# Optimization experiments

Measured on AMD Instinct MI355X. Metric: run time of the kernel, lower is better.

The kernel has to match this reference:

```python
import jax, jax.numpy as jnp
import numpy as np

N, F, H, K_SUB, DEPTH = 500_000, 64, 32, 16, 4
N_NODES = 2 ** DEPTH - 1   # 15 internal nodes
N_LEAVES = 2 ** DEPTH      # 16 leaves
SLOPE = 0.01               # torch LeakyReLU default negative_slope


def _leaky(v):
    return jnp.where(v >= 0, v, SLOPE * v)


def setup_inputs() -> dict:
    key = jax.random.key(0)
    ks = jax.random.split(key, 8)
    x = jax.random.normal(ks[0], (N, F), dtype=jnp.float32)
    subset_idx = jax.random.randint(ks[1], (N_NODES, K_SUB), 0, F, dtype=jnp.int32)
    W1 = jax.random.normal(ks[2], (N_NODES, H, K_SUB), dtype=jnp.float32) * (1.0 / np.sqrt(K_SUB))
    b1 = jnp.zeros((N_NODES, H), jnp.float32)
    W2 = jax.random.normal(ks[3], (N_NODES, H, H), dtype=jnp.float32) * (1.0 / np.sqrt(H))
    b2 = jnp.zeros((N_NODES, H), jnp.float32)
    W3 = jax.random.normal(ks[4], (N_NODES, 2, H), dtype=jnp.float32) * (1.0 / np.sqrt(H))
    b3 = jnp.zeros((N_NODES, 2), jnp.float32)
    # leaf 'best' constants (class modes precomputed by populate_best)
    leaf_best = jax.random.randint(ks[5], (N_LEAVES,), 0, 10).astype(jnp.float32)
    return {"x": x, "W1": W1, "b1": b1, "W2": W2, "b2": b2, "W3": W3, "b3": b3,
            "leaf_best": leaf_best, "subset_idx": subset_idx}


def _forward(x, W1, b1, W2, b2, W3, b3, leaf_best, subset_idx):
    n = x.shape[0]
    loc = jnp.zeros((n,), jnp.int32)   # local node index within current level
    off = 0
    for level in range(DEPTH):
        k = 2 ** level
        sl = slice(off, off + k)
        xs = x[:, subset_idx[sl]]                                   # [N, k, K_SUB]
        h = _leaky(jnp.einsum('nkf,khf->nkh', xs, W1[sl]) + b1[sl])  # [N, k, H]
        h = _leaky(jnp.einsum('nkh,kgh->nkg', h, W2[sl]) + b2[sl])   # [N, k, H]
        logits = jnp.einsum('nkh,koh->nko', h, W3[sl]) + b3[sl]      # [N, k, 2]
        p0 = jax.nn.softmax(logits, axis=-1)[..., 0]                 # [N, k]
        p0_row = jnp.take_along_axis(p0, loc[:, None], axis=1)[:, 0]
        bit = (p0_row < 0.5).astype(jnp.int32)  # 0 -> left, 1 -> right
        loc = 2 * loc + bit
        off += k
    return leaf_best[loc]  # [N]


def reference(x, W1, b1, W2, b2, W3, b3, leaf_best, subset_idx):
    return _forward(x, W1, b1, W2, b2, W3, b3, leaf_best, subset_idx)
```

## Files before the change

kernel.cpp:

```cpp
#include <hip/hip_runtime.h>

#define NF 64
#define NH 32
#define NK 16
#define NNODES 15
#define BLOCK 512
#define NWAVES (BLOCK / 64)
#define SPB (2 * BLOCK)


__global__ __attribute__((amdgpu_flat_work_group_size(BLOCK, BLOCK),
                          amdgpu_waves_per_eu(2, 4)))
void tree_mlp_kernel(
    const float* __restrict__ x,
    const float* __restrict__ W1, const float* __restrict__ b1,
    const float* __restrict__ W2, const float* __restrict__ b2,
    const float* __restrict__ W3, const float* __restrict__ b3,
    const float* __restrict__ leaf_best, const int* __restrict__ subset_idx,
    float* __restrict__ out, int N)
{
    __shared__ __align__(16) float W2Lv[8 * 1024];
    __shared__ int      subL[NNODES * NK];
    __shared__ unsigned permL[SPB];
    __shared__ int      sortL[64];

    const int tid  = threadIdx.x;
    const int lane = tid & 63;
    const int wv   = tid >> 6;
    const unsigned long long lt =
        (lane == 0) ? 0ull : ((~0ull) >> (64 - lane));

    for (int i = tid; i < NNODES * NK; i += BLOCK) subL[i] = subset_idx[i];
    {
        const float4* src = (const float4*)W2;
        float4* dst = (float4*)W2Lv;
        for (int i = tid; i < 256; i += BLOCK) dst[i] = src[i];
    }
    __syncthreads();

    const int base = blockIdx.x * SPB;
    int idA = base + tid;
    int idB = base + BLOCK + tid;
    int vA = (idA < N) ? 1 : 0; if (!vA) idA = 0;
    int vB = (idB < N) ? 1 : 0; if (!vB) idB = 0;
    int locA = 0, locB = 0, off = 0;

    #pragma unroll 1
    for (int level = 0; level < 4; ++level) {
        if (level > 0) {
            const int nb = 1 << level;
            int rkA = 0, rkB = 0;
            #pragma unroll 1
            for (int b = 0; b < nb; ++b) {
                const unsigned long long mA = __ballot(locA == b);
                const unsigned long long mB = __ballot(locB == b);
                if (locA == b) rkA = __popcll(mA & lt);
                if (locB == b) rkB = __popcll(mA) + __popcll(mB & lt);
                if (lane == 0)
                    sortL[b * NWAVES + wv] = __popcll(mA) + __popcll(mB);
            }
            __syncthreads();

            {
                const int cnt4 = (1 << level) * 256;
                const float4* src = (const float4*)(W2 + (size_t)off * 1024);
                float4* dst = (float4*)W2Lv;
                for (int i = tid; i < cnt4; i += BLOCK) dst[i] = src[i];
            }
            if (wv == 0) {
                const int cnt = nb * NWAVES;
                int v = (lane < cnt) ? sortL[lane] : 0;
                int incl = v;
                #pragma unroll
                for (int d = 1; d < 64; d <<= 1) {
                    int t = __shfl_up(incl, d, 64);
                    if (lane >= d) incl += t;
                }
                if (lane < cnt) sortL[lane] = incl - v;
            }
            __syncthreads();

            const int slotA = sortL[locA * NWAVES + wv] + rkA;
            const int slotB = sortL[locB * NWAVES + wv] + rkB;
            permL[slotA] = ((unsigned)idA << 5) | ((unsigned)vA << 4) | (unsigned)locA;
            permL[slotB] = ((unsigned)idB << 5) | ((unsigned)vB << 4) | (unsigned)locB;
            __syncthreads();
            const unsigned pA = permL[wv * 128 + 2 * lane];
            const unsigned pB = permL[wv * 128 + 2 * lane + 1];
            idA = (int)(pA >> 5); vA = (int)((pA >> 4) & 1u); locA = (int)(pA & 15u);
            idB = (int)(pB >> 5); vB = (int)((pB >> 4) & 1u); locB = (int)(pB & 15u);
            __syncthreads();
        }

        const int nodeA = off + locA;
        const int nodeB = off + locB;
        int bitA, bitB;

        if (__all(nodeA == nodeB)) {
            const int* si = subL + nodeA * NK;
            const float* xrA = x + (size_t)idA * NF;
            const float* xrB = x + (size_t)idB * NF;
            float xsA[NK], xsB[NK];
            #pragma unroll
            for (int k = 0; k < NK; ++k) {
                const int f = si[k];
                xsA[k] = xrA[f];
                xsB[k] = xrB[f];
            }

            float h1A[NH], h1B[NH];
            {
                const float4* w1g = (const float4*)(W1 + nodeA * (NH * NK));
                const float*  b1g = b1 + nodeA * NH;
                #pragma unroll
                for (int j = 0; j < NH; ++j) {
                    const float bj = b1g[j];
                    float aA = bj, aB = bj;
                    #pragma unroll
                    for (int q = 0; q < NK / 4; ++q) {
                        const float4 t = w1g[j * 4 + q];
                        aA += t.x * xsA[q * 4 + 0]; aB += t.x * xsB[q * 4 + 0];
                        aA += t.y * xsA[q * 4 + 1]; aB += t.y * xsB[q * 4 + 1];
                        aA += t.z * xsA[q * 4 + 2]; aB += t.z * xsB[q * 4 + 2];
                        aA += t.w * xsA[q * 4 + 3]; aB += t.w * xsB[q * 4 + 3];
                    }
                    h1A[j] = (aA >= 0.f) ? aA : 0.01f * aA;
                    h1B[j] = (aB >= 0.f) ? aB : 0.01f * aB;
                }
            }

            const float* w2l = W2Lv + (locA << 10);
            const float* bb2 = b2 + nodeA * NH;
            const float* w3g = W3 + nodeA * 2 * NH;
            const float bi0 = b3[nodeA * 2 + 0];
            const float bi1 = b3[nodeA * 2 + 1];
            float l0A = bi0, l1A = bi1, l0B = bi0, l1B = bi1;

            #pragma unroll 2
            for (int g = 0; g < NH; ++g) {
                const float bg = bb2[g];
                float aA = bg, aB = bg;
                const float4* row = (const float4*)(w2l + g * NH);
                #pragma unroll
                for (int q = 0; q < NH / 4; ++q) {
                    const float4 t = row[q];
                    aA += t.x * h1A[q * 4 + 0]; aB += t.x * h1B[q * 4 + 0];
                    aA += t.y * h1A[q * 4 + 1]; aB += t.y * h1B[q * 4 + 1];
                    aA += t.z * h1A[q * 4 + 2]; aB += t.z * h1B[q * 4 + 2];
                    aA += t.w * h1A[q * 4 + 3]; aB += t.w * h1B[q * 4 + 3];
                }
                const float h2A = (aA >= 0.f) ? aA : 0.01f * aA;
                const float h2B = (aB >= 0.f) ? aB : 0.01f * aB;
                const float wa = w3g[g];
                const float wb = w3g[NH + g];
                l0A += wa * h2A; l1A += wb * h2A;
                l0B += wa * h2B; l1B += wb * h2B;
            }
            bitA = (l0A < l1A) ? 1 : 0;
            bitB = (l0B < l1B) ? 1 : 0;
        } else {
            #pragma unroll 1
            for (int s2 = 0; s2 < 2; ++s2) {
                const int idS  = s2 ? idB : idA;
                const int locS = s2 ? locB : locA;
                const int node = off + locS;
                const int* si = subL + node * NK;
                const float* xr = x + (size_t)idS * NF;
                float xs[NK];
                #pragma unroll
                for (int k = 0; k < NK; ++k) xs[k] = xr[si[k]];

                float h1v[NH];
                const float4* w1g = (const float4*)(W1 + node * (NH * NK));
                const float*  b1g = b1 + node * NH;
                #pragma unroll
                for (int j = 0; j < NH; ++j) {
                    float acc = b1g[j];
                    #pragma unroll
                    for (int q = 0; q < NK / 4; ++q) {
                        const float4 t = w1g[j * 4 + q];
                        acc += t.x * xs[q * 4 + 0];
                        acc += t.y * xs[q * 4 + 1];
                        acc += t.z * xs[q * 4 + 2];
                        acc += t.w * xs[q * 4 + 3];
                    }
                    h1v[j] = (acc >= 0.f) ? acc : 0.01f * acc;
                }

                const float* w2l = W2Lv + (locS << 10);
                const float* bb2 = b2 + node * NH;
                const float* w3g = W3 + node * 2 * NH;
                float l0 = b3[node * 2 + 0];
                float l1 = b3[node * 2 + 1];
                #pragma unroll 2
                for (int g = 0; g < NH; ++g) {
                    float acc = bb2[g];
                    const float4* row = (const float4*)(w2l + g * NH);
                    #pragma unroll
                    for (int q = 0; q < NH / 4; ++q) {
                        const float4 t = row[q];
                        acc += t.x * h1v[q * 4 + 0];
                        acc += t.y * h1v[q * 4 + 1];
                        acc += t.z * h1v[q * 4 + 2];
                        acc += t.w * h1v[q * 4 + 3];
                    }
                    const float h2 = (acc >= 0.f) ? acc : 0.01f * acc;
                    l0 += w3g[g]      * h2;
                    l1 += w3g[NH + g] * h2;
                }
                const int bit = (l0 < l1) ? 1 : 0;
                if (s2) bitB = bit; else bitA = bit;
            }
        }

        locA = 2 * locA + bitA;
        locB = 2 * locB + bitB;
        off = 2 * off + 1;
    }

    if (vA) out[idA] = leaf_best[locA];
    if (vB) out[idB] = leaf_best[locB];
}

extern "C" void kernel_launch(void* const* d_in, const int* in_sizes, int n_in,
                              void* d_out, int out_size, void* d_ws, size_t ws_size,
                              hipStream_t stream) {
    const float* x         = (const float*)d_in[0];
    const float* W1        = (const float*)d_in[1];
    const float* b1        = (const float*)d_in[2];
    const float* W2        = (const float*)d_in[3];
    const float* b2        = (const float*)d_in[4];
    const float* W3        = (const float*)d_in[5];
    const float* b3        = (const float*)d_in[6];
    const float* leaf_best = (const float*)d_in[7];
    const int*   subset    = (const int*)d_in[8];

    const int N = in_sizes[0] / NF;
    const int grid = (N + SPB - 1) / SPB;
    tree_mlp_kernel<<<grid, BLOCK, 0, stream>>>(
        x, W1, b1, W2, b2, W3, b3, leaf_best, subset, (float*)d_out, N);
}
```

Baseline: 434.3 us.

## Pad per-node sort buckets to even size so sample pairs share a node

Each block now processes 1008 samples instead of 1024. The bucket sort pads every node group to an even length by inserting a dummy slot, so each thread's A/B sample pair always belongs to the same node. This removes the divergent serial fallback path and the per-level __all check, so the paired compute path always runs. In exchange, blocks do slightly less real work, padding slots are computed as invalid samples, and a small extra scan computes the pad offsets.

```diff
diff --git a/kernel.cpp b/kernel.cpp
--- a/kernel.cpp
+++ b/kernel.cpp
@@ -6,7 +6,8 @@
 #define NNODES 15
 #define BLOCK 512
 #define NWAVES (BLOCK / 64)
-#define SPB (2 * BLOCK)
+#define SPB 1008
+#define PSLOTS (1024 + 16)
 
 
 __global__ __attribute__((amdgpu_flat_work_group_size(BLOCK, BLOCK),
@@ -21,8 +22,9 @@
 {
     __shared__ __align__(16) float W2Lv[8 * 1024];
     __shared__ int      subL[NNODES * NK];
-    __shared__ unsigned permL[SPB];
+    __shared__ __align__(8) unsigned permL[PSLOTS];
     __shared__ int      sortL[64];
+    __shared__ int      padL[8];
 
     const int tid  = threadIdx.x;
     const int lane = tid & 63;
@@ -41,21 +43,22 @@
     const int base = blockIdx.x * SPB;
     int idA = base + tid;
     int idB = base + BLOCK + tid;
-    int vA = (idA < N) ? 1 : 0; if (!vA) idA = 0;
-    int vB = (idB < N) ? 1 : 0; if (!vB) idB = 0;
+    int vA = (idA < N) ? 1 : 0;                      if (!vA) idA = 0;
+    int vB = (tid < SPB - BLOCK && idB < N) ? 1 : 0; if (!vB) idB = 0;
     int locA = 0, locB = 0, off = 0;
 
     #pragma unroll 1
     for (int level = 0; level < 4; ++level) {
         if (level > 0) {
             const int nb = 1 << level;
+            *(unsigned long long*)(permL + 2 * tid) = 0ull;
             int rkA = 0, rkB = 0;
             #pragma unroll 1
             for (int b = 0; b < nb; ++b) {
-                const unsigned long long mA = __ballot(locA == b);
-                const unsigned long long mB = __ballot(locB == b);
-                if (locA == b) rkA = __popcll(mA & lt);
-                if (locB == b) rkB = __popcll(mA) + __popcll(mB & lt);
+                const unsigned long long mA = __ballot(vA && locA == b);
+                const unsigned long long mB = __ballot(vB && locB == b);
+                if (vA && locA == b) rkA = __popcll(mA & lt);
+                if (vB && locB == b) rkB = __popcll(mA) + __popcll(mB & lt);
                 if (lane == 0)
                     sortL[b * NWAVES + wv] = __popcll(mA) + __popcll(mB);
             }
@@ -77,27 +80,44 @@
                     if (lane >= d) incl += t;
                 }
                 if (lane < cnt) sortL[lane] = incl - v;
-            }
-            __syncthreads();
-
-            const int slotA = sortL[locA * NWAVES + wv] + rkA;
-            const int slotB = sortL[locB * NWAVES + wv] + rkB;
-            permL[slotA] = ((unsigned)idA << 5) | ((unsigned)vA << 4) | (unsigned)locA;
-            permL[slotB] = ((unsigned)idB << 5) | ((unsigned)vB << 4) | (unsigned)locB;
-            __syncthreads();
-            const unsigned pA = permL[wv * 128 + 2 * lane];
-            const unsigned pB = permL[wv * 128 + 2 * lane + 1];
+                const int iCb = (lane < 8) ? (NWAVES * lane + NWAVES - 1) : 63;
+                const int iCm = (lane >= 1 && lane < 8) ? (NWAVES * lane - 1) : 0;
+                const int Cb    = __shfl(incl, iCb, 64);
+                const int Cm    = __shfl(incl, iCm, 64);
+                const int Cprev = (lane == 0) ? 0 : Cm;
+                const int Tb    = Cb - Cprev;
+                const int odd   = Tb & 1;
+                int po = odd;
+                #pragma unroll
+                for (int d = 1; d < 8; d <<= 1) {
+                    int t = __shfl_up(po, d, 64);
+                    if (lane >= d) po += t;
+                }
+                if (lane < nb) {
+                    const int padb = po - odd;
+                    padL[lane] = padb;
+                    if (odd)
+                        permL[Cprev + padb + Tb] = (unsigned)lane;
+                }
+            }
+            __syncthreads();
+
+            if (vA) permL[sortL[locA * NWAVES + wv] + padL[locA] + rkA]
+                  = ((unsigned)idA << 5) | (1u << 4) | (unsigned)locA;
+            if (vB) permL[sortL[locB * NWAVES + wv] + padL[locB] + rkB]
+                  = ((unsigned)idB << 5) | (1u << 4) | (unsigned)locB;
+            __syncthreads();
+            const unsigned pA = permL[2 * tid];
+            const unsigned pB = permL[2 * tid + 1];
             idA = (int)(pA >> 5); vA = (int)((pA >> 4) & 1u); locA = (int)(pA & 15u);
             idB = (int)(pB >> 5); vB = (int)((pB >> 4) & 1u); locB = (int)(pB & 15u);
             __syncthreads();
         }
 
-        const int nodeA = off + locA;
-        const int nodeB = off + locB;
+        const int node = off + locA;
         int bitA, bitB;
-
-        if (__all(nodeA == nodeB)) {
-            const int* si = subL + nodeA * NK;
+        {
+            const int* si = subL + node * NK;
             const float* xrA = x + (size_t)idA * NF;
             const float* xrB = x + (size_t)idB * NF;
             float xsA[NK], xsB[NK];
@@ -110,8 +130,8 @@
 
             float h1A[NH], h1B[NH];
             {
-                const float4* w1g = (const float4*)(W1 + nodeA * (NH * NK));
-                const float*  b1g = b1 + nodeA * NH;
+                const float4* w1g = (const float4*)(W1 + node * (NH * NK));
+                const float*  b1g = b1 + node * NH;
                 #pragma unroll
                 for (int j = 0; j < NH; ++j) {
                     const float bj = b1g[j];
@@ -130,10 +150,10 @@
             }
 
             const float* w2l = W2Lv + (locA << 10);
-            const float* bb2 = b2 + nodeA * NH;
-            const float* w3g = W3 + nodeA * 2 * NH;
-            const float bi0 = b3[nodeA * 2 + 0];
-            const float bi1 = b3[nodeA * 2 + 1];
+            const float* bb2 = b2 + node * NH;
+            const float* w3g = W3 + node * 2 * NH;
+            const float bi0 = b3[node * 2 + 0];
+            const float bi1 = b3[node * 2 + 1];
             float l0A = bi0, l1A = bi1, l0B = bi0, l1B = bi1;
 
             #pragma unroll 2
@@ -158,59 +178,6 @@
             }
             bitA = (l0A < l1A) ? 1 : 0;
             bitB = (l0B < l1B) ? 1 : 0;
-        } else {
-            #pragma unroll 1
-            for (int s2 = 0; s2 < 2; ++s2) {
-                const int idS  = s2 ? idB : idA;
-                const int locS = s2 ? locB : locA;
-                const int node = off + locS;
-                const int* si = subL + node * NK;
-                const float* xr = x + (size_t)idS * NF;
-                float xs[NK];
-                #pragma unroll
-                for (int k = 0; k < NK; ++k) xs[k] = xr[si[k]];
-
-                float h1v[NH];
-                const float4* w1g = (const float4*)(W1 + node * (NH * NK));
-                const float*  b1g = b1 + node * NH;
-                #pragma unroll
-                for (int j = 0; j < NH; ++j) {
-                    float acc = b1g[j];
-                    #pragma unroll
-                    for (int q = 0; q < NK / 4; ++q) {
-                        const float4 t = w1g[j * 4 + q];
-                        acc += t.x * xs[q * 4 + 0];
-                        acc += t.y * xs[q * 4 + 1];
-                        acc += t.z * xs[q * 4 + 2];
-                        acc += t.w * xs[q * 4 + 3];
-                    }
-                    h1v[j] = (acc >= 0.f) ? acc : 0.01f * acc;
-                }
-
-                const float* w2l = W2Lv + (locS << 10);
-                const float* bb2 = b2 + node * NH;
-                const float* w3g = W3 + node * 2 * NH;
-                float l0 = b3[node * 2 + 0];
-                float l1 = b3[node * 2 + 1];
-                #pragma unroll 2
-                for (int g = 0; g < NH; ++g) {
-                    float acc = bb2[g];
-                    const float4* row = (const float4*)(w2l + g * NH);
-                    #pragma unroll
-                    for (int q = 0; q < NH / 4; ++q) {
-                        const float4 t = row[q];
-                        acc += t.x * h1v[q * 4 + 0];
-                        acc += t.y * h1v[q * 4 + 1];
-                        acc += t.z * h1v[q * 4 + 2];
-                        acc += t.w * h1v[q * 4 + 3];
-                    }
-                    const float h2 = (acc >= 0.f) ? acc : 0.01f * acc;
-                    l0 += w3g[g]      * h2;
-                    l1 += w3g[NH + g] * h2;
-                }
-                const int bit = (l0 < l1) ? 1 : 0;
-                if (s2) bitB = bit; else bitA = bit;
-            }
         }
 
         locA = 2 * locA + bitA;
```

Measured after the change: 438.2 us. About the same (+0.9%).
